# Optimization experiments

Measured on AMD Instinct MI355X. Metric: run time of the kernel, lower is better.

## Reference

```python
import jax, jax.numpy as jnp
import numpy as np
import math

D_MODEL = 1024
NUM_HEADS = 16
D_K = D_MODEL // NUM_HEADS
SEQ = 4096
THETA = 10000.0


def _rope_tables(d_k, max_seq_len, theta):
    freqs = 1.0 / theta ** (jnp.arange(0, d_k, 2, dtype=jnp.float32) / d_k)  # (d_k/2,)
    pos = jnp.arange(max_seq_len, dtype=jnp.float32)
    ang = pos[:, None] * freqs[None, :]  # (S, d_k/2)
    return jnp.cos(ang), jnp.sin(ang)


def setup_inputs() -> dict:
    key = jax.random.key(0)
    ks = jax.random.split(key, 5)
    std = math.sqrt(2.0 / (D_MODEL + D_MODEL))
    def trunc_w(k):
        return jax.random.truncated_normal(k, -3.0, 3.0, (D_MODEL, D_MODEL), jnp.float32) * std
    x = jax.random.normal(ks[0], (1, SEQ, D_MODEL), jnp.float32)
    Wq, Wk, Wv, Wo = trunc_w(ks[1]), trunc_w(ks[2]), trunc_w(ks[3]), trunc_w(ks[4])
    cos, sin = _rope_tables(D_K, SEQ, THETA)
    positions = jnp.arange(SEQ, dtype=jnp.int32)
    return {"x": x, "Wq": Wq, "Wk": Wk, "Wv": Wv, "Wo": Wo,
            "cos": cos, "sin": sin, "positions": positions}


def _apply_rope(t, cos, sin, positions):
    # t: (b, h, s, d_k); cos/sin: (max_s, d_k/2)
    c = cos[positions][None, None]  # (1,1,s,d_k/2)
    s = sin[positions][None, None]
    x1, x2 = t[..., ::2], t[..., 1::2]
    rotated = jnp.stack([x1 * c - x2 * s, x1 * s + x2 * c], axis=-1)  # (b,h,s,d_k/2,2)
    return rotated.reshape(t.shape)


def reference(x, Wq, Wk, Wv, Wo, cos, sin, positions):
    b, s, d = x.shape
    h, dk = NUM_HEADS, D_K
    def proj(W):
        y = jnp.einsum('bsi,oi->bso', x, W)
        return y.reshape(b, s, h, dk).transpose(0, 2, 1, 3)  # (b,h,s,dk)
    Q, K, V = proj(Wq), proj(Wk), proj(Wv)
    Q = _apply_rope(Q, cos, sin, positions)
    K = _apply_rope(K, cos, sin, positions)
    scores = jnp.einsum('bhqd,bhkd->bhqk', Q, K) / math.sqrt(dk)
    causal = jnp.tril(jnp.ones((s, s), dtype=bool))
    scores = jnp.where(causal[None, None], scores, -jnp.inf)
    weights = jax.nn.softmax(scores, axis=-1)
    y = jnp.einsum('bhqk,bhkd->bhqd', weights, V)
    y = y.transpose(0, 2, 1, 3).reshape(b, s, d)
    return jnp.einsum('bsi,oi->bso', y, Wo)
```

## Files before the change

### kernel.cpp

```cpp
#include <hip/hip_runtime.h>
#include <math.h>

#define SEQ 4096
#define DM  1024
#define NH  16
#define DK  64

typedef __attribute__((ext_vector_type(4))) float f32x4;
typedef __attribute__((ext_vector_type(8))) short bf16x8;
typedef __attribute__((ext_vector_type(8))) unsigned short u16x8;

union FragU { u16x8 u; bf16x8 b; ushort4 q[2]; unsigned w[4]; };

__device__ __forceinline__ unsigned cvtpk(float a, float b) {
    unsigned r; asm("v_cvt_pk_bf16_f32 %0, %1, %2" : "=v"(r) : "v"(a), "v"(b)); return r;
}
__device__ __forceinline__ float fexp2(float x) {
    float r; asm("v_exp_f32 %0, %1" : "=v"(r) : "v"(x)); return r;
}
__device__ __forceinline__ void split4(float4 v, ushort4& hv, ushort4& lv) {
    union { ushort4 q; unsigned w[2]; } H, L;
    H.w[0] = cvtpk(v.x, v.y); H.w[1] = cvtpk(v.z, v.w);
    const float rx = v.x - __uint_as_float(H.w[0] << 16);
    const float ry = v.y - __uint_as_float(H.w[0] & 0xffff0000u);
    const float rz = v.z - __uint_as_float(H.w[1] << 16);
    const float rw = v.w - __uint_as_float(H.w[1] & 0xffff0000u);
    L.w[0] = cvtpk(rx, ry); L.w[1] = cvtpk(rz, rw);
    hv = H.q; lv = L.q;
}
__device__ __forceinline__ void split1(float f, unsigned short& h, unsigned short& l) {
    const unsigned hw = cvtpk(f, f) & 0xffffu;
    h = (unsigned short)hw;
    const float r = f - __uint_as_float(hw << 16);
    l = (unsigned short)(__float_as_uint(r) >> 16);
}

template<int MODE>
__global__ __launch_bounds__(256, 2)
void gemm_mfma(const float* __restrict__ Af,
               const unsigned short* __restrict__ Ahi, const unsigned short* __restrict__ Alo,
               const float* __restrict__ W0, const float* __restrict__ W1,
               const float* __restrict__ W2,
               unsigned short* __restrict__ OQh, unsigned short* __restrict__ OQl,
               unsigned short* __restrict__ OKh, unsigned short* __restrict__ OKl,
               unsigned short* __restrict__ OVh, unsigned short* __restrict__ OVl,
               float* __restrict__ Ofp,
               const float* __restrict__ cosT, const float* __restrict__ sinT,
               const int* __restrict__ positions)
{
    constexpr int NT = (MODE == 4) ? 24 : 8;
    __shared__ unsigned short As[128][76];
    __shared__ unsigned short Bs[128][76];

    const int t   = threadIdx.x;
    const int bid = blockIdx.x;
    const int qpx = (32 * NT) >> 3;
    const int swz = (bid & 7) * qpx + (bid >> 3);
    const int by  = swz / NT;
    const int bxf = swz % NT;
    const int wt  = (MODE == 4) ? (bxf >> 3) : 0;
    const int bx  = (MODE == 4) ? (bxf & 7) : bxf;
    const int m0  = by * 128;
    const float* W = (MODE == 4) ? (wt == 0 ? W0 : (wt == 1 ? W1 : W2)) : W0;

    const int lane = t & 63, w = t >> 6;
    const int wr = w >> 1, wc = w & 1;
    const int l15 = lane & 15, lg = lane >> 4;

    const int ar = t >> 1, ah = t & 1;
    const float* Ap = (MODE == 4) ? &Af[(size_t)(m0 + ar) * DM + ah * 16] : nullptr;
    const unsigned short* Aph = (MODE == 0) ? &Ahi[(size_t)(m0 + ar) * DM + ah * 16] : nullptr;
    const unsigned short* Apl = (MODE == 0) ? &Alo[(size_t)(m0 + ar) * DM + ah * 16] : nullptr;
    const float* Wp = &W[(size_t)(bx * 128 + ar) * DM + ah * 16];

    f32x4 acc[4][4];
#pragma unroll
    for (int mi = 0; mi < 4; ++mi)
#pragma unroll
        for (int ni = 0; ni < 4; ++ni) acc[mi][ni] = (f32x4){0.f, 0.f, 0.f, 0.f};

    float4 pa[4], pb[4];
    u16x8 pah[2], pal[2];
    if constexpr (MODE == 4) {
#pragma unroll
        for (int g = 0; g < 4; ++g) pa[g] = *reinterpret_cast<const float4*>(Ap + g * 4);
    } else {
        pah[0] = *reinterpret_cast<const u16x8*>(Aph);
        pah[1] = *reinterpret_cast<const u16x8*>(Aph + 8);
        pal[0] = *reinterpret_cast<const u16x8*>(Apl);
        pal[1] = *reinterpret_cast<const u16x8*>(Apl + 8);
    }
#pragma unroll
    for (int g = 0; g < 4; ++g) pb[g] = *reinterpret_cast<const float4*>(Wp + g * 4);

    for (int kt = 0; kt < 32; ++kt) {
        if constexpr (MODE == 4) {
#pragma unroll
            for (int g = 0; g < 4; ++g) {
                ushort4 hv, lv;
                split4(pa[g], hv, lv);
                *reinterpret_cast<ushort4*>(&As[ar][8 * g + 4 * ah])      = hv;
                *reinterpret_cast<ushort4*>(&As[ar][32 + 8 * g + 4 * ah]) = lv;
            }
        } else {
            FragU h0, h1, l0, l1;
            h0.u = pah[0]; h1.u = pah[1]; l0.u = pal[0]; l1.u = pal[1];
            *reinterpret_cast<ushort4*>(&As[ar][0  + 4 * ah]) = h0.q[0];
            *reinterpret_cast<ushort4*>(&As[ar][8  + 4 * ah]) = h0.q[1];
            *reinterpret_cast<ushort4*>(&As[ar][16 + 4 * ah]) = h1.q[0];
            *reinterpret_cast<ushort4*>(&As[ar][24 + 4 * ah]) = h1.q[1];
            *reinterpret_cast<ushort4*>(&As[ar][32 + 4 * ah]) = l0.q[0];
            *reinterpret_cast<ushort4*>(&As[ar][40 + 4 * ah]) = l0.q[1];
            *reinterpret_cast<ushort4*>(&As[ar][48 + 4 * ah]) = l1.q[0];
            *reinterpret_cast<ushort4*>(&As[ar][56 + 4 * ah]) = l1.q[1];
        }
#pragma unroll
        for (int g = 0; g < 4; ++g) {
            ushort4 hv, lv;
            split4(pb[g], hv, lv);
            *reinterpret_cast<ushort4*>(&Bs[ar][8 * g + 4 * ah])      = hv;
            *reinterpret_cast<ushort4*>(&Bs[ar][32 + 8 * g + 4 * ah]) = lv;
        }
        __syncthreads();

        if (kt < 31) {
            const int ko = (kt + 1) * 32;
            if constexpr (MODE == 4) {
#pragma unroll
                for (int g = 0; g < 4; ++g)
                    pa[g] = *reinterpret_cast<const float4*>(Ap + ko + g * 4);
            } else {
                pah[0] = *reinterpret_cast<const u16x8*>(Aph + ko);
                pah[1] = *reinterpret_cast<const u16x8*>(Aph + ko + 8);
                pal[0] = *reinterpret_cast<const u16x8*>(Apl + ko);
                pal[1] = *reinterpret_cast<const u16x8*>(Apl + ko + 8);
            }
#pragma unroll
            for (int g = 0; g < 4; ++g)
                pb[g] = *reinterpret_cast<const float4*>(Wp + ko + g * 4);
        }

        FragU b_h[4], b_l[4];
#pragma unroll
        for (int ni = 0; ni < 4; ++ni) {
            const int row = wc * 64 + ni * 16 + l15;
            b_h[ni].u = *reinterpret_cast<const u16x8*>(&Bs[row][8 * lg]);
            b_l[ni].u = *reinterpret_cast<const u16x8*>(&Bs[row][32 + 8 * lg]);
        }
#pragma unroll
        for (int mi = 0; mi < 4; ++mi) {
            FragU a_h, a_l;
            const int row = wr * 64 + mi * 16 + l15;
            a_h.u = *reinterpret_cast<const u16x8*>(&As[row][8 * lg]);
            a_l.u = *reinterpret_cast<const u16x8*>(&As[row][32 + 8 * lg]);
#pragma unroll
            for (int ni = 0; ni < 4; ++ni) {
                f32x4 c = acc[mi][ni];
                c = __builtin_amdgcn_mfma_f32_16x16x32_bf16(a_h.b, b_h[ni].b, c, 0, 0, 0);
                c = __builtin_amdgcn_mfma_f32_16x16x32_bf16(a_h.b, b_l[ni].b, c, 0, 0, 0);
                c = __builtin_amdgcn_mfma_f32_16x16x32_bf16(a_l.b, b_h[ni].b, c, 0, 0, 0);
                acc[mi][ni] = c;
            }
        }
        __syncthreads();
    }

    if constexpr (MODE == 0) {
#pragma unroll
        for (int mi = 0; mi < 4; ++mi)
#pragma unroll
            for (int ni = 0; ni < 4; ++ni)
#pragma unroll
                for (int r = 0; r < 4; ++r) {
                    const int m = m0 + wr * 64 + mi * 16 + lg * 4 + r;
                    const int n = bx * 128 + wc * 64 + ni * 16 + l15;
                    Ofp[(size_t)m * DM + n] = acc[mi][ni][r];
                }
    } else if (wt == 2) {
#pragma unroll
        for (int mi = 0; mi < 4; ++mi)
#pragma unroll
            for (int ni = 0; ni < 4; ++ni) {
                ushort4 hv, lv;
                unsigned short* hp = (unsigned short*)&hv;
                unsigned short* lp = (unsigned short*)&lv;
#pragma unroll
                for (int r = 0; r < 4; ++r) split1(acc[mi][ni][r], hp[r], lp[r]);
                const int vrow = bx * 128 + wc * 64 + ni * 16 + l15;
                const size_t off = (size_t)vrow * SEQ + m0 + wr * 64 + mi * 16 + lg * 4;
                *reinterpret_cast<ushort4*>(&OVh[off]) = hv;
                *reinterpret_cast<ushort4*>(&OVl[off]) = lv;
            }
    } else {
        unsigned short* Oh = (wt == 0) ? OQh : OKh;
        unsigned short* Ol = (wt == 0) ? OQl : OKl;
        const int head = bx * 2 + wc;
        const float qsc = 0.1803368801f;
#pragma unroll
        for (int mi = 0; mi < 4; ++mi)
#pragma unroll
            for (int r = 0; r < 4; ++r) {
                const int m   = m0 + wr * 64 + mi * 16 + lg * 4 + r;
                const int pos = positions[m];
#pragma unroll
                for (int ni = 0; ni < 4; ++ni) {
                    float val = acc[mi][ni][r];
                    const int d = ni * 16 + l15;
                    const float other = __shfl_xor(val, 1);
                    const float cc = cosT[pos * 32 + ni * 8 + (l15 >> 1)];
                    const float ss = sinT[pos * 32 + ni * 8 + (l15 >> 1)];
                    val = (d & 1) ? fmaf(other, ss, val * cc)
                                  : fmaf(other, -ss, val * cc);
                    if (wt == 0) val *= qsc;
                    unsigned short hh, ll;
                    split1(val, hh, ll);
                    const size_t off = ((size_t)head * SEQ + m) * DK + d;
                    Oh[off] = hh; Ol[off] = ll;
                }
            }
    }
}

__global__ __launch_bounds__(256, 2)
void attn_mfma(const unsigned short* __restrict__ Qhi, const unsigned short* __restrict__ Qlo,
               const unsigned short* __restrict__ Khi, const unsigned short* __restrict__ Klo,
               const unsigned short* __restrict__ Vhi,
               unsigned short* __restrict__ Yh, unsigned short* __restrict__ Yl)
{
    __shared__ unsigned short KsH[64][64], KsL[64][64], Vs[64][64];

    const int t = threadIdx.x, lane = t & 63, w = t >> 6;
    const int bid = blockIdx.x;
    const int xcd = bid & 7;
    const int s   = bid >> 3;
    const int i_  = s >> 1, hl = s & 1;
    const int A   = (i_ < 16) ? i_ : 47 - i_;
    const int qt  = hl ? (31 - A) : A;
    const int h   = 2 * xcd + hl;

    const int l15 = lane & 15, lg = lane >> 4, dg = lg * 4;
    const int srow = t >> 2, q16 = t & 3;
    const int wh = w & 1;

    int wcol[4];
#pragma unroll
    for (int m = 0; m < 4; ++m) {
        const int g = (q16 >> 1) * 4 + m;
        wcol[m] = (((g ^ (srow & 7)) << 3) + ((q16 & 1) << 2));
    }

    const int NKT    = 2 * qt + 2;
    const int diagkt = 2 * qt + (w >> 1);

    bf16x8 qh[2][2], ql[2][2];
#pragma unroll
    for (int u = 0; u < 2; ++u) {
        const size_t qrow = ((size_t)h * SEQ + (size_t)qt * 128 + w * 32 + u * 16 + l15) * DK;
#pragma unroll
        for (int c = 0; c < 2; ++c) {
            FragU uh, ul;
            uh.q[0] = *reinterpret_cast<const ushort4*>(&Qhi[qrow + c * 32 + dg]);
            uh.q[1] = *reinterpret_cast<const ushort4*>(&Qhi[qrow + c * 32 + 16 + dg]);
            ul.q[0] = *reinterpret_cast<const ushort4*>(&Qlo[qrow + c * 32 + dg]);
            ul.q[1] = *reinterpret_cast<const ushort4*>(&Qlo[qrow + c * 32 + 16 + dg]);
            qh[u][c] = uh.b; ql[u][c] = ul.b;
        }
    }

    f32x4 yacc[2][4];
#pragma unroll
    for (int u = 0; u < 2; ++u)
#pragma unroll
        for (int dt = 0; dt < 4; ++dt) yacc[u][dt] = (f32x4){0.f, 0.f, 0.f, 0.f};
    float m_run[2] = {-1e30f, -1e30f}, l_run[2] = {0.f, 0.f};

    u16x8 pf[6];
    {
        const size_t gK = ((size_t)h * SEQ + srow) * DK + q16 * 16;
        const size_t gV = ((size_t)h * DK + srow) * SEQ + q16 * 16;
        pf[0] = *reinterpret_cast<const u16x8*>(&Khi[gK]);
        pf[1] = *reinterpret_cast<const u16x8*>(&Khi[gK + 8]);
        pf[2] = *reinterpret_cast<const u16x8*>(&Klo[gK]);
        pf[3] = *reinterpret_cast<const u16x8*>(&Klo[gK + 8]);
        pf[4] = *reinterpret_cast<const u16x8*>(&Vhi[gV]);
        pf[5] = *reinterpret_cast<const u16x8*>(&Vhi[gV + 8]);
    }

    for (int kt = 0; kt < NKT; ++kt) {
        __syncthreads();
        {
            FragU f;
            f.u = pf[0];
            *reinterpret_cast<ushort4*>(&KsH[srow][wcol[0]]) = f.q[0];
            *reinterpret_cast<ushort4*>(&KsH[srow][wcol[1]]) = f.q[1];
            f.u = pf[1];
            *reinterpret_cast<ushort4*>(&KsH[srow][wcol[2]]) = f.q[0];
            *reinterpret_cast<ushort4*>(&KsH[srow][wcol[3]]) = f.q[1];
            f.u = pf[2];
            *reinterpret_cast<ushort4*>(&KsL[srow][wcol[0]]) = f.q[0];
            *reinterpret_cast<ushort4*>(&KsL[srow][wcol[1]]) = f.q[1];
            f.u = pf[3];
            *reinterpret_cast<ushort4*>(&KsL[srow][wcol[2]]) = f.q[0];
            *reinterpret_cast<ushort4*>(&KsL[srow][wcol[3]]) = f.q[1];
            f.u = pf[4];
            *reinterpret_cast<ushort4*>(&Vs[srow][wcol[0]]) = f.q[0];
            *reinterpret_cast<ushort4*>(&Vs[srow][wcol[1]]) = f.q[1];
            f.u = pf[5];
            *reinterpret_cast<ushort4*>(&Vs[srow][wcol[2]]) = f.q[0];
            *reinterpret_cast<ushort4*>(&Vs[srow][wcol[3]]) = f.q[1];
        }
        __syncthreads();

        if (kt + 1 < NKT) {
            const size_t gK = ((size_t)h * SEQ + (size_t)(kt + 1) * 64 + srow) * DK + q16 * 16;
            const size_t gV = ((size_t)h * DK + srow) * SEQ + (size_t)(kt + 1) * 64 + q16 * 16;
            pf[0] = *reinterpret_cast<const u16x8*>(&Khi[gK]);
            pf[1] = *reinterpret_cast<const u16x8*>(&Khi[gK + 8]);
            pf[2] = *reinterpret_cast<const u16x8*>(&Klo[gK]);
            pf[3] = *reinterpret_cast<const u16x8*>(&Klo[gK + 8]);
            pf[4] = *reinterpret_cast<const u16x8*>(&Vhi[gV]);
            pf[5] = *reinterpret_cast<const u16x8*>(&Vhi[gV + 8]);
        }

        if (kt > diagkt) continue;
        const bool diag = (kt == diagkt);

        f32x4 st[2][4];
        __builtin_amdgcn_s_setprio(1);
#pragma unroll
        for (int ktile = 0; ktile < 4; ++ktile) {
            const int rowK = ktile * 16 + l15;
            const int swk  = rowK & 7;
            FragU kh0, kl0, kh1, kl1;
            {
                const int p0 = ((0 + lg) ^ swk) << 3;
                const int p1 = ((4 + lg) ^ swk) << 3;
                kh0.u = *reinterpret_cast<const u16x8*>(&KsH[rowK][p0]);
                kl0.u = *reinterpret_cast<const u16x8*>(&KsL[rowK][p0]);
                kh1.u = *reinterpret_cast<const u16x8*>(&KsH[rowK][p1]);
                kl1.u = *reinterpret_cast<const u16x8*>(&KsL[rowK][p1]);
            }
#pragma unroll
            for (int u = 0; u < 2; ++u) {
                if (diag && ktile > wh * 2 + u) {
                    st[u][ktile] = (f32x4){-1e30f, -1e30f, -1e30f, -1e30f};
                    continue;
                }
                f32x4 s0 = (f32x4){0.f, 0.f, 0.f, 0.f};
                s0 = __builtin_amdgcn_mfma_f32_16x16x32_bf16(kh0.b, qh[u][0], s0, 0, 0, 0);
                s0 = __builtin_amdgcn_mfma_f32_16x16x32_bf16(kh0.b, ql[u][0], s0, 0, 0, 0);
                s0 = __builtin_amdgcn_mfma_f32_16x16x32_bf16(kl0.b, qh[u][0], s0, 0, 0, 0);
                s0 = __builtin_amdgcn_mfma_f32_16x16x32_bf16(kh1.b, qh[u][1], s0, 0, 0, 0);
                s0 = __builtin_amdgcn_mfma_f32_16x16x32_bf16(kh1.b, ql[u][1], s0, 0, 0, 0);
                s0 = __builtin_amdgcn_mfma_f32_16x16x32_bf16(kl1.b, qh[u][1], s0, 0, 0, 0);
                st[u][ktile] = s0;
            }
        }
        __builtin_amdgcn_s_setprio(0);

        if (diag) {
#pragma unroll
            for (int u = 0; u < 2; ++u) {
                const int ub = wh * 2 + u;
#pragma unroll
                for (int r = 0; r < 4; ++r)
                    if (dg + r > l15) st[u][ub][r] = -1e30f;
            }
        }

        bf16x8 pa[2][2];
#pragma unroll
        for (int u = 0; u < 2; ++u) {
            float rowmax = st[u][0][0];
#pragma unroll
            for (int ktile = 0; ktile < 4; ++ktile)
#pragma unroll
                for (int r = 0; r < 4; ++r) rowmax = fmaxf(rowmax, st[u][ktile][r]);
            rowmax = fmaxf(rowmax, __shfl_xor(rowmax, 16));
            rowmax = fmaxf(rowmax, __shfl_xor(rowmax, 32));
            if (!__all(rowmax <= m_run[u] + 11.5f)) {
                const float mnew = fmaxf(m_run[u], rowmax);
                const float factor = fexp2(m_run[u] - mnew);
                l_run[u] *= factor;
#pragma unroll
                for (int r = 0; r < 4; ++r) {
                    const float fr = __shfl(factor, (lg << 2) | r);
#pragma unroll
                    for (int dt = 0; dt < 4; ++dt) yacc[u][dt][r] *= fr;
                }
                m_run[u] = mnew;
            }
            float p[4][4]; float psum = 0.f;
#pragma unroll
            for (int ktile = 0; ktile < 4; ++ktile)
#pragma unroll
                for (int r = 0; r < 4; ++r) {
                    p[ktile][r] = fexp2(st[u][ktile][r] - m_run[u]);
                    psum += p[ktile][r];
                }
            psum += __shfl_xor(psum, 16);
            psum += __shfl_xor(psum, 32);
            l_run[u] += psum;
#pragma unroll
            for (int c = 0; c < 2; ++c) {
                FragU P;
                P.w[0] = cvtpk(p[2 * c][0],     p[2 * c][1]);
                P.w[1] = cvtpk(p[2 * c][2],     p[2 * c][3]);
                P.w[2] = cvtpk(p[2 * c + 1][0], p[2 * c + 1][1]);
                P.w[3] = cvtpk(p[2 * c + 1][2], p[2 * c + 1][3]);
                pa[u][c] = P.b;
            }
        }

        __builtin_amdgcn_s_setprio(1);
#pragma unroll
        for (int dt = 0; dt < 4; ++dt) {
            const int rowV = dt * 16 + l15;
            const int swv  = rowV & 7;
#pragma unroll
            for (int c = 0; c < 2; ++c) {
                FragU vh;
                vh.u = *reinterpret_cast<const u16x8*>(&Vs[rowV][((c * 4 + lg) ^ swv) << 3]);
#pragma unroll
                for (int u = 0; u < 2; ++u) {
                    if (diag && c == 1 && (wh * 2 + u) < 2) continue;
                    yacc[u][dt] = __builtin_amdgcn_mfma_f32_16x16x32_bf16(pa[u][c], vh.b, yacc[u][dt], 0, 0, 0);
                }
            }
        }
        __builtin_amdgcn_s_setprio(0);
    }

#pragma unroll
    for (int u = 0; u < 2; ++u) {
        const float inv = 1.0f / l_run[u];
#pragma unroll
        for (int r = 0; r < 4; ++r) {
            const float ir = __shfl(inv, (lg << 2) | r);
            const size_t row = (size_t)qt * 128 + w * 32 + u * 16 + lg * 4 + r;
#pragma unroll
            for (int dt = 0; dt < 4; ++dt) {
                unsigned short hh, ll;
                split1(yacc[u][dt][r] * ir, hh, ll);
                const size_t off = row * DM + h * DK + dt * 16 + l15;
                Yh[off] = hh; Yl[off] = ll;
            }
        }
    }
}

extern "C" void kernel_launch(void* const* d_in, const int* in_sizes, int n_in,
                              void* d_out, int out_size, void* d_ws, size_t ws_size,
                              hipStream_t stream)
{
    const float* x    = (const float*)d_in[0];
    const float* Wq   = (const float*)d_in[1];
    const float* Wk   = (const float*)d_in[2];
    const float* Wv   = (const float*)d_in[3];
    const float* Wo   = (const float*)d_in[4];
    const float* cosT = (const float*)d_in[5];
    const float* sinT = (const float*)d_in[6];
    const int*   pos  = (const int*)d_in[7];
    float* out = (float*)d_out;

    const size_t E = (size_t)SEQ * DM;
    unsigned short* qh = (unsigned short*)d_ws;
    unsigned short* ql = qh + E;
    unsigned short* kh = ql + E;
    unsigned short* kl = kh + E;
    unsigned short* vh = kl + E;
    unsigned short* vl = vh + E;
    unsigned short* yh = vl + E;
    unsigned short* yl = yh + E;

    gemm_mfma<4><<<dim3(768), dim3(256), 0, stream>>>(
        x, nullptr, nullptr, Wq, Wk, Wv,
        qh, ql, kh, kl, vh, vl, nullptr, cosT, sinT, pos);
    attn_mfma<<<dim3(512), dim3(256), 0, stream>>>(qh, ql, kh, kl, vh, yh, yl);
    gemm_mfma<0><<<dim3(256), dim3(256), 0, stream>>>(
        nullptr, yh, yl, Wo, nullptr, nullptr,
        nullptr, nullptr, nullptr, nullptr, nullptr, nullptr, out, cosT, sinT, pos);
}
```

Before: 291.6 us.

## Split heavy causal query tiles across blocks with split-K and merge kernel

Attention work is rebalanced. Half the blocks process a light query tile plus the first half of a heavy tile's key range. The other half process the second half of that heavy tile's key range. Partial outputs plus running max and sum are written out, and a new merge kernel combines them with log-sum-exp rescaling. This targets load imbalance across blocks from the causal triangle. The cost is an extra kernel launch, extra global traffic for the partials, and bf16-only storage of one partial. Separately, the unused V low-precision split store is dropped from the projection GEMM.

```diff
diff --git a/kernel.cpp b/kernel.cpp
--- a/kernel.cpp
+++ b/kernel.cpp
@@ -17,6 +17,9 @@
 }
 __device__ __forceinline__ float fexp2(float x) {
     float r; asm("v_exp_f32 %0, %1" : "=v"(r) : "v"(x)); return r;
+}
+__device__ __forceinline__ float bf_f(unsigned short s) {
+    return __uint_as_float(((unsigned)s) << 16);
 }
 __device__ __forceinline__ void split4(float4 v, ushort4& hv, ushort4& lv) {
     union { ushort4 q; unsigned w[2]; } H, L;
@@ -43,7 +46,7 @@
                const float* __restrict__ W2,
                unsigned short* __restrict__ OQh, unsigned short* __restrict__ OQl,
                unsigned short* __restrict__ OKh, unsigned short* __restrict__ OKl,
-               unsigned short* __restrict__ OVh, unsigned short* __restrict__ OVl,
+               unsigned short* __restrict__ OVh,
                float* __restrict__ Ofp,
                const float* __restrict__ cosT, const float* __restrict__ sinT,
                const int* __restrict__ positions)
@@ -181,15 +184,14 @@
         for (int mi = 0; mi < 4; ++mi)
 #pragma unroll
             for (int ni = 0; ni < 4; ++ni) {
-                ushort4 hv, lv;
-                unsigned short* hp = (unsigned short*)&hv;
-                unsigned short* lp = (unsigned short*)&lv;
-#pragma unroll
-                for (int r = 0; r < 4; ++r) split1(acc[mi][ni][r], hp[r], lp[r]);
+                ushort4 hv;
+                unsigned short* hp_ = (unsigned short*)&hv;
+#pragma unroll
+                for (int r = 0; r < 4; ++r)
+                    hp_[r] = (unsigned short)(cvtpk(acc[mi][ni][r], acc[mi][ni][r]) & 0xffffu);
                 const int vrow = bx * 128 + wc * 64 + ni * 16 + l15;
                 const size_t off = (size_t)vrow * SEQ + m0 + wr * 64 + mi * 16 + lg * 4;
                 *reinterpret_cast<ushort4*>(&OVh[off]) = hv;
-                *reinterpret_cast<ushort4*>(&OVl[off]) = lv;
             }
     } else {
         unsigned short* Oh = (wt == 0) ? OQh : OKh;
@@ -225,18 +227,21 @@
 void attn_mfma(const unsigned short* __restrict__ Qhi, const unsigned short* __restrict__ Qlo,
                const unsigned short* __restrict__ Khi, const unsigned short* __restrict__ Klo,
                const unsigned short* __restrict__ Vhi,
-               unsigned short* __restrict__ Yh, unsigned short* __restrict__ Yl)
+               unsigned short* __restrict__ Yh, unsigned short* __restrict__ Yl,
+               unsigned short* __restrict__ Pb,
+               float2* __restrict__ mlA, float2* __restrict__ mlB)
 {
     __shared__ unsigned short KsH[64][64], KsL[64][64], Vs[64][64];
 
     const int t = threadIdx.x, lane = t & 63, w = t >> 6;
-    const int bid = blockIdx.x;
-    const int xcd = bid & 7;
-    const int s   = bid >> 3;
-    const int i_  = s >> 1, hl = s & 1;
-    const int A   = (i_ < 16) ? i_ : 47 - i_;
-    const int qt  = hl ? (31 - A) : A;
-    const int h   = 2 * xcd + hl;
+    const int bid  = blockIdx.x;
+    const int xcd  = bid & 7;
+    const int s    = bid >> 3;
+    const int hl   = s & 1;
+    const int slot = s >> 1;
+    const int p    = slot & 15;
+    const int half = slot >> 4;
+    const int h    = 2 * xcd + hl;
 
     const int l15 = lane & 15, lg = lane >> 4, dg = lg * 4;
     const int srow = t >> 2, q16 = t & 3;
@@ -249,203 +254,277 @@
         wcol[m] = (((g ^ (srow & 7)) << 3) + ((q16 & 1) << 2));
     }
 
-    const int NKT    = 2 * qt + 2;
-    const int diagkt = 2 * qt + (w >> 1);
-
-    bf16x8 qh[2][2], ql[2][2];
-#pragma unroll
-    for (int u = 0; u < 2; ++u) {
-        const size_t qrow = ((size_t)h * SEQ + (size_t)qt * 128 + w * 32 + u * 16 + l15) * DK;
-#pragma unroll
-        for (int c = 0; c < 2; ++c) {
-            FragU uh, ul;
-            uh.q[0] = *reinterpret_cast<const ushort4*>(&Qhi[qrow + c * 32 + dg]);
-            uh.q[1] = *reinterpret_cast<const ushort4*>(&Qhi[qrow + c * 32 + 16 + dg]);
-            ul.q[0] = *reinterpret_cast<const ushort4*>(&Qlo[qrow + c * 32 + dg]);
-            ul.q[1] = *reinterpret_cast<const ushort4*>(&Qlo[qrow + c * 32 + 16 + dg]);
-            qh[u][c] = uh.b; ql[u][c] = ul.b;
-        }
-    }
-
-    f32x4 yacc[2][4];
-#pragma unroll
-    for (int u = 0; u < 2; ++u)
-#pragma unroll
-        for (int dt = 0; dt < 4; ++dt) yacc[u][dt] = (f32x4){0.f, 0.f, 0.f, 0.f};
-    float m_run[2] = {-1e30f, -1e30f}, l_run[2] = {0.f, 0.f};
-
     u16x8 pf[6];
-    {
-        const size_t gK = ((size_t)h * SEQ + srow) * DK + q16 * 16;
-        const size_t gV = ((size_t)h * DK + srow) * SEQ + q16 * 16;
+    auto PREFETCH = [&](int ktn) {
+        const size_t gK = ((size_t)h * SEQ + (size_t)ktn * 64 + srow) * DK + q16 * 16;
+        const size_t gV = ((size_t)h * DK + srow) * SEQ + (size_t)ktn * 64 + q16 * 16;
         pf[0] = *reinterpret_cast<const u16x8*>(&Khi[gK]);
         pf[1] = *reinterpret_cast<const u16x8*>(&Khi[gK + 8]);
         pf[2] = *reinterpret_cast<const u16x8*>(&Klo[gK]);
         pf[3] = *reinterpret_cast<const u16x8*>(&Klo[gK + 8]);
         pf[4] = *reinterpret_cast<const u16x8*>(&Vhi[gV]);
         pf[5] = *reinterpret_cast<const u16x8*>(&Vhi[gV + 8]);
+    };
+
+    const int nph = (half == 0) ? 2 : 1;
+#pragma unroll 1
+    for (int ph = 0; ph < nph; ++ph) {
+        const int qt    = (half == 0 && ph == 0) ? p : (31 - p);
+        const int kt0   = (half == 1) ? (31 - 2 * p) : 0;
+        const int kt1   = (half == 0) ? ((ph == 0) ? (2 * p + 2) : (31 - 2 * p))
+                                      : (64 - 2 * p);
+        const int emode = (half == 0) ? ph : 2;
+        const int diagkt = 2 * qt + (w >> 1);
+
+        bf16x8 qh[2][2], ql[2][2];
+#pragma unroll
+        for (int u = 0; u < 2; ++u) {
+            const size_t qrow = ((size_t)h * SEQ + (size_t)qt * 128 + w * 32 + u * 16 + l15) * DK;
+#pragma unroll
+            for (int c = 0; c < 2; ++c) {
+                FragU uh, ul;
+                uh.q[0] = *reinterpret_cast<const ushort4*>(&Qhi[qrow + c * 32 + dg]);
+                uh.q[1] = *reinterpret_cast<const ushort4*>(&Qhi[qrow + c * 32 + 16 + dg]);
+                ul.q[0] = *reinterpret_cast<const ushort4*>(&Qlo[qrow + c * 32 + dg]);
+                ul.q[1] = *reinterpret_cast<const ushort4*>(&Qlo[qrow + c * 32 + 16 + dg]);
+                qh[u][c] = uh.b; ql[u][c] = ul.b;
+            }
+        }
+
+        f32x4 yacc[2][4];
+#pragma unroll
+        for (int u = 0; u < 2; ++u)
+#pragma unroll
+            for (int dt = 0; dt < 4; ++dt) yacc[u][dt] = (f32x4){0.f, 0.f, 0.f, 0.f};
+        float m_run[2] = {-1e30f, -1e30f}, l_run[2] = {0.f, 0.f};
+
+        PREFETCH(kt0);
+
+        for (int kt = kt0; kt < kt1; ++kt) {
+            __syncthreads();
+            {
+                FragU f;
+                f.u = pf[0];
+                *reinterpret_cast<ushort4*>(&KsH[srow][wcol[0]]) = f.q[0];
+                *reinterpret_cast<ushort4*>(&KsH[srow][wcol[1]]) = f.q[1];
+                f.u = pf[1];
+                *reinterpret_cast<ushort4*>(&KsH[srow][wcol[2]]) = f.q[0];
+                *reinterpret_cast<ushort4*>(&KsH[srow][wcol[3]]) = f.q[1];
+                f.u = pf[2];
+                *reinterpret_cast<ushort4*>(&KsL[srow][wcol[0]]) = f.q[0];
+                *reinterpret_cast<ushort4*>(&KsL[srow][wcol[1]]) = f.q[1];
+                f.u = pf[3];
+                *reinterpret_cast<ushort4*>(&KsL[srow][wcol[2]]) = f.q[0];
+                *reinterpret_cast<ushort4*>(&KsL[srow][wcol[3]]) = f.q[1];
+                f.u = pf[4];
+                *reinterpret_cast<ushort4*>(&Vs[srow][wcol[0]]) = f.q[0];
+                *reinterpret_cast<ushort4*>(&Vs[srow][wcol[1]]) = f.q[1];
+                f.u = pf[5];
+                *reinterpret_cast<ushort4*>(&Vs[srow][wcol[2]]) = f.q[0];
+                *reinterpret_cast<ushort4*>(&Vs[srow][wcol[3]]) = f.q[1];
+            }
+            __syncthreads();
+
+            if (kt + 1 < kt1) PREFETCH(kt + 1);
+
+            if (kt > diagkt) continue;
+            const bool diag = (kt == diagkt);
+
+            f32x4 st[2][4];
+            __builtin_amdgcn_s_setprio(1);
+#pragma unroll
+            for (int ktile = 0; ktile < 4; ++ktile) {
+                const int rowK = ktile * 16 + l15;
+                const int swk  = rowK & 7;
+                FragU kh0, kl0, kh1, kl1;
+                {
+                    const int p0 = ((0 + lg) ^ swk) << 3;
+                    const int p1 = ((4 + lg) ^ swk) << 3;
+                    kh0.u = *reinterpret_cast<const u16x8*>(&KsH[rowK][p0]);
+                    kl0.u = *reinterpret_cast<const u16x8*>(&KsL[rowK][p0]);
+                    kh1.u = *reinterpret_cast<const u16x8*>(&KsH[rowK][p1]);
+                    kl1.u = *reinterpret_cast<const u16x8*>(&KsL[rowK][p1]);
+                }
+#pragma unroll
+                for (int u = 0; u < 2; ++u) {
+                    if (diag && ktile > wh * 2 + u) {
+                        st[u][ktile] = (f32x4){-1e30f, -1e30f, -1e30f, -1e30f};
+                        continue;
+                    }
+                    f32x4 s0 = (f32x4){0.f, 0.f, 0.f, 0.f};
+                    s0 = __builtin_amdgcn_mfma_f32_16x16x32_bf16(kh0.b, qh[u][0], s0, 0, 0, 0);
+                    s0 = __builtin_amdgcn_mfma_f32_16x16x32_bf16(kh0.b, ql[u][0], s0, 0, 0, 0);
+                    s0 = __builtin_amdgcn_mfma_f32_16x16x32_bf16(kl0.b, qh[u][0], s0, 0, 0, 0);
+                    s0 = __builtin_amdgcn_mfma_f32_16x16x32_bf16(kh1.b, qh[u][1], s0, 0, 0, 0);
+                    s0 = __builtin_amdgcn_mfma_f32_16x16x32_bf16(kh1.b, ql[u][1], s0, 0, 0, 0);
+                    s0 = __builtin_amdgcn_mfma_f32_16x16x32_bf16(kl1.b, qh[u][1], s0, 0, 0, 0);
+                    st[u][ktile] = s0;
+                }
+            }
+            __builtin_amdgcn_s_setprio(0);
+
+            if (diag) {
+#pragma unroll
+                for (int u = 0; u < 2; ++u) {
+                    const int ub = wh * 2 + u;
+#pragma unroll
+                    for (int r = 0; r < 4; ++r)
+                        if (dg + r > l15) st[u][ub][r] = -1e30f;
+                }
+            }
+
+            bf16x8 pa[2][2];
+#pragma unroll
+            for (int u = 0; u < 2; ++u) {
+                float rowmax = st[u][0][0];
+#pragma unroll
+                for (int ktile = 0; ktile < 4; ++ktile)
+#pragma unroll
+                    for (int r = 0; r < 4; ++r) rowmax = fmaxf(rowmax, st[u][ktile][r]);
+                rowmax = fmaxf(rowmax, __shfl_xor(rowmax, 16));
+                rowmax = fmaxf(rowmax, __shfl_xor(rowmax, 32));
+                if (!__all(rowmax <= m_run[u] + 11.5f)) {
+                    const float mnew = fmaxf(m_run[u], rowmax);
+                    const float factor = fexp2(m_run[u] - mnew);
+                    l_run[u] *= factor;
+#pragma unroll
+                    for (int r = 0; r < 4; ++r) {
+                        const float fr = __shfl(factor, (lg << 2) | r);
+#pragma unroll
+                        for (int dt = 0; dt < 4; ++dt) yacc[u][dt][r] *= fr;
+                    }
+                    m_run[u] = mnew;
+                }
+                float pp[4][4]; float psum = 0.f;
+#pragma unroll
+                for (int ktile = 0; ktile < 4; ++ktile)
+#pragma unroll
+                    for (int r = 0; r < 4; ++r) {
+                        pp[ktile][r] = fexp2(st[u][ktile][r] - m_run[u]);
+                        psum += pp[ktile][r];
+                    }
+                psum += __shfl_xor(psum, 16);
+                psum += __shfl_xor(psum, 32);
+                l_run[u] += psum;
+#pragma unroll
+                for (int c = 0; c < 2; ++c) {
+                    FragU P;
+                    P.w[0] = cvtpk(pp[2 * c][0],     pp[2 * c][1]);
+                    P.w[1] = cvtpk(pp[2 * c][2],     pp[2 * c][3]);
+                    P.w[2] = cvtpk(pp[2 * c + 1][0], pp[2 * c + 1][1]);
+                    P.w[3] = cvtpk(pp[2 * c + 1][2], pp[2 * c + 1][3]);
+                    pa[u][c] = P.b;
+                }
+            }
+
+            __builtin_amdgcn_s_setprio(1);
+#pragma unroll
+            for (int dt = 0; dt < 4; ++dt) {
+                const int rowV = dt * 16 + l15;
+                const int swv  = rowV & 7;
+#pragma unroll
+                for (int c = 0; c < 2; ++c) {
+                    FragU vh;
+                    vh.u = *reinterpret_cast<const u16x8*>(&Vs[rowV][((c * 4 + lg) ^ swv) << 3]);
+#pragma unroll
+                    for (int u = 0; u < 2; ++u) {
+                        if (diag && c == 1 && (wh * 2 + u) < 2) continue;
+                        yacc[u][dt] = __builtin_amdgcn_mfma_f32_16x16x32_bf16(pa[u][c], vh.b, yacc[u][dt], 0, 0, 0);
+                    }
+                }
+            }
+            __builtin_amdgcn_s_setprio(0);
+        }
+
+        if (emode == 0) {
+#pragma unroll
+            for (int u = 0; u < 2; ++u) {
+                const float inv = 1.0f / l_run[u];
+#pragma unroll
+                for (int r = 0; r < 4; ++r) {
+                    const float ir = __shfl(inv, (lg << 2) | r);
+                    const size_t row = (size_t)qt * 128 + w * 32 + u * 16 + lg * 4 + r;
+#pragma unroll
+                    for (int dt = 0; dt < 4; ++dt) {
+                        unsigned short hh, ll;
+                        split1(yacc[u][dt][r] * ir, hh, ll);
+                        const size_t off = row * DM + h * DK + dt * 16 + l15;
+                        Yh[off] = hh; Yl[off] = ll;
+                    }
+                }
+            }
+        } else if (emode == 1) {
+#pragma unroll
+            for (int u = 0; u < 2; ++u) {
+#pragma unroll
+                for (int r = 0; r < 4; ++r) {
+                    const size_t row = (size_t)qt * 128 + w * 32 + u * 16 + lg * 4 + r;
+#pragma unroll
+                    for (int dt = 0; dt < 4; ++dt) {
+                        unsigned short hh, ll;
+                        split1(yacc[u][dt][r], hh, ll);
+                        const size_t off = row * DM + h * DK + dt * 16 + l15;
+                        Yh[off] = hh; Yl[off] = ll;
+                    }
+                }
+                if (lane < 16)
+                    mlA[(h * 16 + p) * 128 + w * 32 + u * 16 + lane] =
+                        make_float2(m_run[u], l_run[u]);
+            }
+        } else {
+#pragma unroll
+            for (int u = 0; u < 2; ++u) {
+#pragma unroll
+                for (int r = 0; r < 4; ++r) {
+                    const int rloc = w * 32 + u * 16 + lg * 4 + r;
+#pragma unroll
+                    for (int dt = 0; dt < 4; ++dt) {
+                        Pb[((size_t)(h * 16 + p) * 128 + rloc) * 64 + dt * 16 + l15] =
+                            (unsigned short)(cvtpk(yacc[u][dt][r], yacc[u][dt][r]) & 0xffffu);
+                    }
+                }
+                if (lane < 16)
+                    mlB[(h * 16 + p) * 128 + w * 32 + u * 16 + lane] =
+                        make_float2(m_run[u], l_run[u]);
+            }
+        }
     }
-
-    for (int kt = 0; kt < NKT; ++kt) {
-        __syncthreads();
-        {
-            FragU f;
-            f.u = pf[0];
-            *reinterpret_cast<ushort4*>(&KsH[srow][wcol[0]]) = f.q[0];
-            *reinterpret_cast<ushort4*>(&KsH[srow][wcol[1]]) = f.q[1];
-            f.u = pf[1];
-            *reinterpret_cast<ushort4*>(&KsH[srow][wcol[2]]) = f.q[0];
-            *reinterpret_cast<ushort4*>(&KsH[srow][wcol[3]]) = f.q[1];
-            f.u = pf[2];
-            *reinterpret_cast<ushort4*>(&KsL[srow][wcol[0]]) = f.q[0];
-            *reinterpret_cast<ushort4*>(&KsL[srow][wcol[1]]) = f.q[1];
-            f.u = pf[3];
-            *reinterpret_cast<ushort4*>(&KsL[srow][wcol[2]]) = f.q[0];
-            *reinterpret_cast<ushort4*>(&KsL[srow][wcol[3]]) = f.q[1];
-            f.u = pf[4];
-            *reinterpret_cast<ushort4*>(&Vs[srow][wcol[0]]) = f.q[0];
-            *reinterpret_cast<ushort4*>(&Vs[srow][wcol[1]]) = f.q[1];
-            f.u = pf[5];
-            *reinterpret_cast<ushort4*>(&Vs[srow][wcol[2]]) = f.q[0];
-            *reinterpret_cast<ushort4*>(&Vs[srow][wcol[3]]) = f.q[1];
-        }
-        __syncthreads();
-
-        if (kt + 1 < NKT) {
-            const size_t gK = ((size_t)h * SEQ + (size_t)(kt + 1) * 64 + srow) * DK + q16 * 16;
-            const size_t gV = ((size_t)h * DK + srow) * SEQ + (size_t)(kt + 1) * 64 + q16 * 16;
-            pf[0] = *reinterpret_cast<const u16x8*>(&Khi[gK]);
-            pf[1] = *reinterpret_cast<const u16x8*>(&Khi[gK + 8]);
-            pf[2] = *reinterpret_cast<const u16x8*>(&Klo[gK]);
-            pf[3] = *reinterpret_cast<const u16x8*>(&Klo[gK + 8]);
-            pf[4] = *reinterpret_cast<const u16x8*>(&Vhi[gV]);
-            pf[5] = *reinterpret_cast<const u16x8*>(&Vhi[gV + 8]);
-        }
-
-        if (kt > diagkt) continue;
-        const bool diag = (kt == diagkt);
-
-        f32x4 st[2][4];
-        __builtin_amdgcn_s_setprio(1);
-#pragma unroll
-        for (int ktile = 0; ktile < 4; ++ktile) {
-            const int rowK = ktile * 16 + l15;
-            const int swk  = rowK & 7;
-            FragU kh0, kl0, kh1, kl1;
-            {
-                const int p0 = ((0 + lg) ^ swk) << 3;
-                const int p1 = ((4 + lg) ^ swk) << 3;
-                kh0.u = *reinterpret_cast<const u16x8*>(&KsH[rowK][p0]);
-                kl0.u = *reinterpret_cast<const u16x8*>(&KsL[rowK][p0]);
-                kh1.u = *reinterpret_cast<const u16x8*>(&KsH[rowK][p1]);
-                kl1.u = *reinterpret_cast<const u16x8*>(&KsL[rowK][p1]);
-            }
-#pragma unroll
-            for (int u = 0; u < 2; ++u) {
-                if (diag && ktile > wh * 2 + u) {
-                    st[u][ktile] = (f32x4){-1e30f, -1e30f, -1e30f, -1e30f};
-                    continue;
-                }
-                f32x4 s0 = (f32x4){0.f, 0.f, 0.f, 0.f};
-                s0 = __builtin_amdgcn_mfma_f32_16x16x32_bf16(kh0.b, qh[u][0], s0, 0, 0, 0);
-                s0 = __builtin_amdgcn_mfma_f32_16x16x32_bf16(kh0.b, ql[u][0], s0, 0, 0, 0);
-                s0 = __builtin_amdgcn_mfma_f32_16x16x32_bf16(kl0.b, qh[u][0], s0, 0, 0, 0);
-                s0 = __builtin_amdgcn_mfma_f32_16x16x32_bf16(kh1.b, qh[u][1], s0, 0, 0, 0);
-                s0 = __builtin_amdgcn_mfma_f32_16x16x32_bf16(kh1.b, ql[u][1], s0, 0, 0, 0);
-                s0 = __builtin_amdgcn_mfma_f32_16x16x32_bf16(kl1.b, qh[u][1], s0, 0, 0, 0);
-                st[u][ktile] = s0;
-            }
-        }
-        __builtin_amdgcn_s_setprio(0);
-
-        if (diag) {
-#pragma unroll
-            for (int u = 0; u < 2; ++u) {
-                const int ub = wh * 2 + u;
-#pragma unroll
-                for (int r = 0; r < 4; ++r)
-                    if (dg + r > l15) st[u][ub][r] = -1e30f;
-            }
-        }
-
-        bf16x8 pa[2][2];
-#pragma unroll
-        for (int u = 0; u < 2; ++u) {
-            float rowmax = st[u][0][0];
-#pragma unroll
-            for (int ktile = 0; ktile < 4; ++ktile)
-#pragma unroll
-                for (int r = 0; r < 4; ++r) rowmax = fmaxf(rowmax, st[u][ktile][r]);
-            rowmax = fmaxf(rowmax, __shfl_xor(rowmax, 16));
-            rowmax = fmaxf(rowmax, __shfl_xor(rowmax, 32));
-            if (!__all(rowmax <= m_run[u] + 11.5f)) {
-                const float mnew = fmaxf(m_run[u], rowmax);
-                const float factor = fexp2(m_run[u] - mnew);
-                l_run[u] *= factor;
-#pragma unroll
-                for (int r = 0; r < 4; ++r) {
-                    const float fr = __shfl(factor, (lg << 2) | r);
-#pragma unroll
-                    for (int dt = 0; dt < 4; ++dt) yacc[u][dt][r] *= fr;
-                }
-                m_run[u] = mnew;
-            }
-            float p[4][4]; float psum = 0.f;
-#pragma unroll
-            for (int ktile = 0; ktile < 4; ++ktile)
-#pragma unroll
-                for (int r = 0; r < 4; ++r) {
-                    p[ktile][r] = fexp2(st[u][ktile][r] - m_run[u]);
-                    psum += p[ktile][r];
-                }
-            psum += __shfl_xor(psum, 16);
-            psum += __shfl_xor(psum, 32);
-            l_run[u] += psum;
-#pragma unroll
-            for (int c = 0; c < 2; ++c) {
-                FragU P;
-                P.w[0] = cvtpk(p[2 * c][0],     p[2 * c][1]);
-                P.w[1] = cvtpk(p[2 * c][2],     p[2 * c][3]);
-                P.w[2] = cvtpk(p[2 * c + 1][0], p[2 * c + 1][1]);
-                P.w[3] = cvtpk(p[2 * c + 1][2], p[2 * c + 1][3]);
-                pa[u][c] = P.b;
-            }
-        }
-
-        __builtin_amdgcn_s_setprio(1);
-#pragma unroll
-        for (int dt = 0; dt < 4; ++dt) {
-            const int rowV = dt * 16 + l15;
-            const int swv  = rowV & 7;
-#pragma unroll
-            for (int c = 0; c < 2; ++c) {
-                FragU vh;
-                vh.u = *reinterpret_cast<const u16x8*>(&Vs[rowV][((c * 4 + lg) ^ swv) << 3]);
-#pragma unroll
-                for (int u = 0; u < 2; ++u) {
-                    if (diag && c == 1 && (wh * 2 + u) < 2) continue;
-                    yacc[u][dt] = __builtin_amdgcn_mfma_f32_16x16x32_bf16(pa[u][c], vh.b, yacc[u][dt], 0, 0, 0);
-                }
-            }
-        }
-        __builtin_amdgcn_s_setprio(0);
-    }
-
-#pragma unroll
-    for (int u = 0; u < 2; ++u) {
-        const float inv = 1.0f / l_run[u];
-#pragma unroll
-        for (int r = 0; r < 4; ++r) {
-            const float ir = __shfl(inv, (lg << 2) | r);
-            const size_t row = (size_t)qt * 128 + w * 32 + u * 16 + lg * 4 + r;
-#pragma unroll
-            for (int dt = 0; dt < 4; ++dt) {
-                unsigned short hh, ll;
-                split1(yacc[u][dt][r] * ir, hh, ll);
-                const size_t off = row * DM + h * DK + dt * 16 + l15;
-                Yh[off] = hh; Yl[off] = ll;
-            }
-        }
+}
+
+__global__ __launch_bounds__(256)
+void merge_heavy(unsigned short* __restrict__ Yh, unsigned short* __restrict__ Yl,
+                 const unsigned short* __restrict__ Pb,
+                 const float2* __restrict__ mlA, const float2* __restrict__ mlB)
+{
+    const int hp = blockIdx.x;
+    const int h = hp >> 4, p = hp & 15;
+    const int t = threadIdx.x;
+    const int row = t >> 1;
+    const int d0 = (t & 1) * 32;
+    const float2 a = mlA[hp * 128 + row];
+    const float2 b = mlB[hp * 128 + row];
+    const float m  = fmaxf(a.x, b.x);
+    const float fA = fexp2(a.x - m), fB = fexp2(b.x - m);
+    const float inv = 1.0f / (fA * a.y + fB * b.y);
+    const size_t rg = ((size_t)(31 - p) * 128 + row) * DM + h * DK + d0;
+    const size_t pg = ((size_t)hp * 128 + row) * 64 + d0;
+#pragma unroll
+    for (int dd = 0; dd < 32; dd += 8) {
+        u16x8 vh = *reinterpret_cast<const u16x8*>(&Yh[rg + dd]);
+        u16x8 vl = *reinterpret_cast<const u16x8*>(&Yl[rg + dd]);
+        u16x8 vb = *reinterpret_cast<const u16x8*>(&Pb[pg + dd]);
+        u16x8 oh, ol;
+#pragma unroll
+        for (int j = 0; j < 8; ++j) {
+            const float ya = bf_f(vh[j]) + bf_f(vl[j]);
+            const float yb = bf_f(vb[j]);
+            const float o  = (fA * ya + fB * yb) * inv;
+            unsigned short hh, ll;
+            split1(o, hh, ll);
+            oh[j] = hh; ol[j] = ll;
+        }
+        *reinterpret_cast<u16x8*>(&Yh[rg + dd]) = oh;
+        *reinterpret_cast<u16x8*>(&Yl[rg + dd]) = ol;
     }
 }
 
@@ -469,15 +548,19 @@
     unsigned short* kh = ql + E;
     unsigned short* kl = kh + E;
     unsigned short* vh = kl + E;
-    unsigned short* vl = vh + E;
-    unsigned short* yh = vl + E;
+    unsigned short* yh = vh + E;
     unsigned short* yl = yh + E;
+    unsigned short* Pb = yl + E;
+    float2* mlA = (float2*)(Pb + (size_t)256 * 128 * 64);
+    float2* mlB = mlA + (size_t)256 * 128;
 
     gemm_mfma<4><<<dim3(768), dim3(256), 0, stream>>>(
         x, nullptr, nullptr, Wq, Wk, Wv,
-        qh, ql, kh, kl, vh, vl, nullptr, cosT, sinT, pos);
-    attn_mfma<<<dim3(512), dim3(256), 0, stream>>>(qh, ql, kh, kl, vh, yh, yl);
+        qh, ql, kh, kl, vh, nullptr, cosT, sinT, pos);
+    attn_mfma<<<dim3(512), dim3(256), 0, stream>>>(
+        qh, ql, kh, kl, vh, yh, yl, Pb, mlA, mlB);
+    merge_heavy<<<dim3(256), dim3(256), 0, stream>>>(yh, yl, Pb, mlA, mlB);
     gemm_mfma<0><<<dim3(256), dim3(256), 0, stream>>>(
         nullptr, yh, yl, Wo, nullptr, nullptr,
-        nullptr, nullptr, nullptr, nullptr, nullptr, nullptr, out, cosT, sinT, pos);
-}
+        nullptr, nullptr, nullptr, nullptr, nullptr, out, cosT, sinT, pos);
+}
```

New measurement: 273.2 us. 1.07x faster.
